# Performance work log

Hardware: AMD Instinct MI355X
Metric: run time of the kernel (lower is better)

## Reference

```python
import jax, jax.numpy as jnp
import numpy as np

SUB_NO = 128
T_HIST = 100
T_DATA = 20000
SYN_B = 3
HIST_B = 3
FIX_VAR = 1.0


def _build_kern(delta, log_tau, K):
    # delta: (S,), log_tau: (B,), K: (S,B) -> kernel (S, T_HIST)
    t = jnp.maximum(jnp.arange(T_HIST, dtype=jnp.float32)[None, :] - delta[:, None], 0.0)  # (S,T)
    tt = t[:, :, None] / jnp.exp(log_tau)[None, None, :]  # (S,T,B)
    return jnp.einsum('stb,sb->st', tt * jnp.exp(-tt), K)


def setup_inputs() -> dict:
    key = jax.random.key(0)
    ks = jax.random.split(key, 5)
    S = SUB_NO
    return {
        'S_conv': jax.random.normal(ks[0], (T_DATA, S), jnp.float32),
        'Y_ancest': jax.random.normal(ks[1], (T_DATA, S), jnp.float32),
        'Z_ancest': jax.random.uniform(ks[2], (T_DATA, S), jnp.float32),
        'noise': jax.random.normal(ks[3], (T_DATA, S), jnp.float32),
        'C_den': jax.random.uniform(ks[4], (S, S), jnp.float32),
        'W_sub': jnp.ones(S, jnp.float32) * 0.25,
        'theta_syn': jnp.zeros(S, jnp.float32),
        'K_spike': jnp.ones((S, SYN_B), jnp.float32) * 0.01,
        'tau_spike': jnp.arange(1.6, 1.6 + SYN_B, dtype=jnp.float32),
        'delta_spike': jnp.zeros(S, jnp.float32),
        'theta_spike': jnp.ones(S, jnp.float32) * (-1.0),
        'W_spike': jnp.ones(S, jnp.float32) * 0.1,
        'tau_hist': jnp.arange(0.5, 0.5 + HIST_B * 0.5, 0.5, dtype=jnp.float32),
        'K_hist': jnp.zeros((S, HIST_B), jnp.float32),
        'delta_hist': jnp.zeros(S, jnp.float32),
    }


def _forward(S_conv, Y_ancest, Z_ancest, noise, C_den, W_sub, theta_syn,
             K_spike, tau_spike, delta_spike, theta_spike, W_spike,
             tau_hist, K_hist, delta_hist):
    S = SUB_NO
    # kernels, flipped as in torch (conv1d cross-correlation with flipped kernel)
    hist_kf = _build_kern(delta_hist, tau_hist, K_hist)[:, ::-1]      # (S,T_HIST)
    anc_kf = _build_kern(delta_spike, tau_spike, K_spike)[:, ::-1]    # (S,T_HIST)

    # Ancestor path has no recurrence -> hoist out of the time loop.
    # spike_ancest filtering: C_den is linear & time-independent, so project first,
    # then depthwise-convolve along time.
    Z_pad = jnp.concatenate([jnp.zeros((T_HIST, S), S_conv.dtype), Z_ancest], axis=0)  # (T+T_HIST,S)
    A = Z_pad @ C_den.T  # (T+T_HIST, S)
    conv = jax.lax.conv_general_dilated(
        A.T[None],                 # (1, S, T+T_HIST)
        anc_kf[:, None, :],        # (S, 1, T_HIST)
        window_strides=(1,), padding='VALID',
        dimension_numbers=('NCH', 'OIH', 'NCH'),
        feature_group_count=S)     # (1, S, T_DATA+1)
    filtered_ancest = conv[0].T[:T_DATA]  # (T_DATA, S)

    raw_ancest = Y_ancest @ C_den.T  # (T_DATA, S)
    base = S_conv + theta_syn + filtered_ancest + raw_ancest  # (T_DATA,S)
    sqrt_var = FIX_VAR ** 0.5

    def step(buf, inp):
        # buf: (S, T_HIST) rolling history of Z_out (most recent at index -1)
        b, n = inp
        fh = jnp.sum(buf * hist_kf, axis=1)            # grouped conv1d == per-channel dot
        x_out = jax.nn.sigmoid(b + fh)
        down = x_out * W_spike + theta_spike           # down_mu_Z_t == mu_Z_t (up_mu_Z=None)
        z_out = jax.nn.sigmoid(down + n * sqrt_var)
        buf = jnp.concatenate([buf[:, 1:], z_out[:, None]], axis=1)
        return buf, (x_out * W_sub, z_out, down)

    buf0 = jnp.zeros((S, T_HIST), S_conv.dtype)
    _, (final_Y, final_Z, mu_Z) = jax.lax.scan(step, buf0, (base, noise))
    return final_Y, final_Z, mu_Z, mu_Z


def reference(S_conv, Y_ancest, Z_ancest, noise, C_den, W_sub, theta_syn,
              K_spike, tau_spike, delta_spike, theta_spike, W_spike,
              tau_hist, K_hist, delta_hist):
    return _forward(S_conv, Y_ancest, Z_ancest, noise, C_den, W_sub, theta_syn,
                    K_spike, tau_spike, delta_spike, theta_spike, W_spike,
                    tau_hist, K_hist, delta_hist)
```

## Files before the change

### kernel.cpp

```cpp
#include <hip/hip_runtime.h>

#define T_DATA 20000
#define S_NO   128
#define T_HIST 100
#define J_PAD  104
#define NELEM  (T_DATA * S_NO)

__device__ __forceinline__ float sigm(float v) {
    return 1.0f / (1.0f + __expf(-v));
}

__device__ __forceinline__ void fma4(float4& a, float s, const float4 c) {
    a.x = fmaf(s, c.x, a.x); a.y = fmaf(s, c.y, a.y);
    a.z = fmaf(s, c.z, a.z); a.w = fmaf(s, c.w, a.w);
}

__global__ void __launch_bounds__(256) k1_prep(const float* __restrict__ C,
                        const float* __restrict__ K_spike,
                        const float* __restrict__ tau_spike,
                        const float* __restrict__ delta_spike,
                        const float* __restrict__ tau_hist,
                        const float* __restrict__ K_hist,
                        const float* __restrict__ delta_hist,
                        float* __restrict__ Ct,
                        float* __restrict__ anc_kT,
                        float* __restrict__ hist_k,
                        int* __restrict__ flag) {
    const int tid = threadIdx.x;
    const int b   = blockIdx.x;
    if (b < 16) {
#pragma unroll
        for (int i = 0; i < 4; ++i) {
            const int q = b * 1024 + i * 256 + tid;
            Ct[(q & 127) * S_NO + (q >> 7)] = C[q];
        }
        return;
    }
    const int s    = tid & 127;
    const int half = tid >> 7;
    {
        float d  = delta_spike[s];
        float i0 = __expf(-tau_spike[0]);
        float i1 = __expf(-tau_spike[1]);
        float i2 = __expf(-tau_spike[2]);
        float k0 = K_spike[s * 3 + 0], k1 = K_spike[s * 3 + 1], k2 = K_spike[s * 3 + 2];
        for (int j = half * 52; j < half * 52 + 52; ++j) {
            float v = 0.0f;
            if (j < T_HIST) {
                float t  = fmaxf((float)j - d, 0.0f);
                float x0 = t * i0, x1 = t * i1, x2 = t * i2;
                v = k0 * x0 * __expf(-x0) + k1 * x1 * __expf(-x1) + k2 * x2 * __expf(-x2);
            }
            anc_kT[j * S_NO + s] = v;
        }
    }
    {
        float d  = delta_hist[s];
        float i0 = __expf(-tau_hist[0]);
        float i1 = __expf(-tau_hist[1]);
        float i2 = __expf(-tau_hist[2]);
        float k0 = K_hist[s * 3 + 0], k1 = K_hist[s * 3 + 1], k2 = K_hist[s * 3 + 2];
        for (int j = half * 50; j < half * 50 + 50; ++j) {
            float t  = fmaxf((float)j - d, 0.0f);
            float x0 = t * i0, x1 = t * i1, x2 = t * i2;
            hist_k[s * T_HIST + j] =
                k0 * x0 * __expf(-x0) + k1 * x1 * __expf(-x1) + k2 * x2 * __expf(-x2);
        }
    }
    if (tid == 0) *flag = 0;
    __syncthreads();
    if (tid < 128) {
        if (K_hist[s * 3] != 0.0f || K_hist[s * 3 + 1] != 0.0f || K_hist[s * 3 + 2] != 0.0f)
            atomicOr(flag, 1);
    }
}

__global__ void __launch_bounds__(256) k2_gemm(const float* __restrict__ Z,
                                               const float* __restrict__ Y,
                                               const float* __restrict__ Ct,
                                               float* __restrict__ A,
                                               float* __restrict__ R) {
    __shared__ float Zt[32 * 128];
    __shared__ float Yt[32 * 128];
    const int t0  = blockIdx.x * 32;
    const int tid = threadIdx.x;
    {
        const float4* Zg = (const float4*)(Z + t0 * S_NO);
        const float4* Yg = (const float4*)(Y + t0 * S_NO);
        float4* Zl = (float4*)Zt;
        float4* Yl = (float4*)Yt;
        for (int q = tid; q < 1024; q += 256) { Zl[q] = Zg[q]; Yl[q] = Yg[q]; }
    }
    __syncthreads();
    const int sg = tid & 31;
    const int tg = tid >> 5;
    const int s0 = sg * 4;
    float4 accA[4] = {{0,0,0,0},{0,0,0,0},{0,0,0,0},{0,0,0,0}};
    float4 accR[4] = {{0,0,0,0},{0,0,0,0},{0,0,0,0},{0,0,0,0}};
    for (int k4 = 0; k4 < 32; ++k4) {
        const float4 c0 = *(const float4*)&Ct[(k4 * 4 + 0) * S_NO + s0];
        const float4 c1 = *(const float4*)&Ct[(k4 * 4 + 1) * S_NO + s0];
        const float4 c2 = *(const float4*)&Ct[(k4 * 4 + 2) * S_NO + s0];
        const float4 c3 = *(const float4*)&Ct[(k4 * 4 + 3) * S_NO + s0];
#pragma unroll
        for (int i = 0; i < 4; ++i) {
            const float4 z = *(const float4*)&Zt[(tg * 4 + i) * S_NO + k4 * 4];
            fma4(accA[i], z.x, c0); fma4(accA[i], z.y, c1);
            fma4(accA[i], z.z, c2); fma4(accA[i], z.w, c3);
            const float4 y = *(const float4*)&Yt[(tg * 4 + i) * S_NO + k4 * 4];
            fma4(accR[i], y.x, c0); fma4(accR[i], y.y, c1);
            fma4(accR[i], y.z, c2); fma4(accR[i], y.w, c3);
        }
    }
#pragma unroll
    for (int i = 0; i < 4; ++i) {
        *(float4*)&A[(t0 + tg * 4 + i) * S_NO + s0] = accA[i];
        *(float4*)&R[(t0 + tg * 4 + i) * S_NO + s0] = accR[i];
    }
}

#define K3_LOGICAL 1250
#define K3_NPER    157
#define K3_PHYS    (8 * K3_NPER)

__device__ __forceinline__ void k3_load_chunk(const float* __restrict__ A,
                                              const float* __restrict__ kT,
                                              int t0, int s, int c,
                                              float w[15], float kj[8]) {
    const int B = t0 - 8 * c - 8;
#pragma unroll
    for (int q = 0; q < 15; ++q) w[q] = A[(B + q) * S_NO + s];
#pragma unroll
    for (int r = 0; r < 8; ++r) kj[r] = kT[(8 * c + r) * S_NO + s];
}

__device__ __forceinline__ void k3_fma_chunk(const float w[15], const float kj[8],
                                             float acc[8]) {
#pragma unroll
    for (int r = 0; r < 8; ++r)
#pragma unroll
        for (int i = 0; i < 8; ++i)
            acc[i] = fmaf(kj[r], w[i + 7 - r], acc[i]);
}

__device__ __forceinline__ void conv8_guard(const float* __restrict__ A,
                                            const float* __restrict__ kT,
                                            int t0, int s, float acc[8]) {
#pragma unroll 1
    for (int c = 0; c < 13; ++c) {
        const int B = t0 - 8 * c - 8;
        float w[15], kj[8];
#pragma unroll
        for (int q = 0; q < 15; ++q) {
            const int u = B + q;
            w[q] = (u >= 0) ? A[u * S_NO + s] : 0.0f;
        }
#pragma unroll
        for (int r = 0; r < 8; ++r) kj[r] = kT[(8 * c + r) * S_NO + s];
        k3_fma_chunk(w, kj, acc);
    }
}

__global__ void __launch_bounds__(256, 4) k3_fused(const float* __restrict__ A,
                                                const float* __restrict__ anc_kT,
                                                const float* __restrict__ S_conv,
                                                const float* __restrict__ noise,
                                                const float* __restrict__ W_sub,
                                                const float* __restrict__ theta_syn,
                                                const float* __restrict__ theta_spike,
                                                const float* __restrict__ W_spike,
                                                const int* __restrict__ flag,
                                                float* __restrict__ out0,
                                                float* __restrict__ out1,
                                                float* __restrict__ out2,
                                                float* __restrict__ out3,
                                                float* __restrict__ Fws) {
    const int blk = (blockIdx.x & 7) * K3_NPER + (blockIdx.x >> 3);
    if (blk >= K3_LOGICAL) return;
    const int tid = threadIdx.x;
    const int s   = tid & 127;
    const int tg  = tid >> 7;
    const int t0  = blk * 16 + tg * 8;
    const int fl  = *flag;

    float sc[8], nz[8];
#pragma unroll
    for (int i = 0; i < 8; ++i) {
        const int n = (t0 + i) * S_NO + s;
        sc[i] = S_conv[n];
        nz[i] = noise[n];
    }

    float acc[8] = {0,0,0,0,0,0,0,0};
    if (t0 >= J_PAD) {
        float w0[15], k0[8], w1[15], k1[8];
        k3_load_chunk(A, anc_kT, t0, s, 0, w0, k0);
#pragma unroll 1
        for (int c = 0; c < 12; c += 2) {
            k3_load_chunk(A, anc_kT, t0, s, c + 1, w1, k1);
            k3_fma_chunk(w0, k0, acc);
            k3_load_chunk(A, anc_kT, t0, s, c + 2, w0, k0);
            k3_fma_chunk(w1, k1, acc);
        }
        k3_fma_chunk(w0, k0, acc);
    } else {
        conv8_guard(A, anc_kT, t0, s, acc);
    }

    if (fl == 0) {
        const float tsy = theta_syn[s], wsub = W_sub[s];
        const float wsp = W_spike[s],  tsp  = theta_spike[s];
#pragma unroll
        for (int i = 0; i < 8; ++i) {
            const int n = (t0 + i) * S_NO + s;
            const float x  = sigm(sc[i] + tsy + out1[n] + acc[i]);
            const float dn = fmaf(x, wsp, tsp);
            const float z  = sigm(dn + nz[i]);
            out0[n] = x * wsub;
            out1[n] = z;
            out2[n] = dn;
            out3[n] = dn;
        }
    } else {
#pragma unroll
        for (int i = 0; i < 8; ++i) Fws[(t0 + i) * S_NO + s] = acc[i];
    }
}

__global__ void __launch_bounds__(64) k4_scan(const float* __restrict__ S_conv,
                                              const float* __restrict__ noise,
                                              const float* __restrict__ W_sub,
                                              const float* __restrict__ theta_syn,
                                              const float* __restrict__ theta_spike,
                                              const float* __restrict__ W_spike,
                                              const float* __restrict__ hist_k,
                                              const int* __restrict__ flag,
                                              const float* __restrict__ Fws,
                                              float* __restrict__ out0,
                                              float* __restrict__ out1,
                                              float* __restrict__ out2,
                                              float* __restrict__ out3) {
    if (*flag == 0) return;
    __shared__ float zr[128];
    const int s = blockIdx.x;
    const int l = threadIdx.x;
    zr[l] = 0.0f; zr[l + 64] = 0.0f;
    const float hk0 = (l < T_HIST) ? hist_k[s * T_HIST + l] : 0.0f;
    const float hk1 = (l + 64 < T_HIST) ? hist_k[s * T_HIST + l + 64] : 0.0f;
    const float tsy = theta_syn[s], wsub = W_sub[s];
    const float wsp = W_spike[s],  tsp  = theta_spike[s];
    for (int t = 0; t < T_DATA; ++t) {
        float fh = hk0 * zr[(t - 1 - l) & 127];
        fh = fmaf(hk1, zr[(t - 65 - l) & 127], fh);
#pragma unroll
        for (int m = 1; m < 64; m <<= 1) fh += __shfl_xor(fh, m, 64);
        const int n = t * S_NO + s;
        const float basev = S_conv[n] + tsy + out1[n] + Fws[n];
        const float x  = sigm(basev + fh);
        const float dn = fmaf(x, wsp, tsp);
        const float z  = sigm(dn + noise[n]);
        if (l == 0) {
            out0[n] = x * wsub;
            out1[n] = z;
            out2[n] = dn;
            out3[n] = dn;
            zr[t & 127] = z;
        }
    }
}

extern "C" void kernel_launch(void* const* d_in, const int* in_sizes, int n_in,
                              void* d_out, int out_size, void* d_ws, size_t ws_size,
                              hipStream_t stream) {
    const float* S_conv  = (const float*)d_in[0];
    const float* Y_anc   = (const float*)d_in[1];
    const float* Z_anc   = (const float*)d_in[2];
    const float* noise   = (const float*)d_in[3];
    const float* C_den   = (const float*)d_in[4];
    const float* W_sub   = (const float*)d_in[5];
    const float* th_syn  = (const float*)d_in[6];
    const float* K_spk   = (const float*)d_in[7];
    const float* tau_spk = (const float*)d_in[8];
    const float* dl_spk  = (const float*)d_in[9];
    const float* th_spk  = (const float*)d_in[10];
    const float* W_spk   = (const float*)d_in[11];
    const float* tau_h   = (const float*)d_in[12];
    const float* K_h     = (const float*)d_in[13];
    const float* dl_h    = (const float*)d_in[14];

    float* out  = (float*)d_out;
    float* out0 = out;
    float* out1 = out + NELEM;
    float* out2 = out + 2 * NELEM;
    float* out3 = out + 3 * NELEM;

    float* ws     = (float*)d_ws;
    float* wsA    = ws;
    float* wsF    = ws + NELEM;
    float* Ct     = ws + 2 * NELEM;
    float* anc_kT = Ct + S_NO * S_NO;
    float* hist_k = anc_kT + J_PAD * S_NO;
    int*   flag   = (int*)(hist_k + S_NO * T_HIST);

    k1_prep<<<17, 256, 0, stream>>>(C_den, K_spk, tau_spk, dl_spk, tau_h, K_h, dl_h,
                                    Ct, anc_kT, hist_k, flag);
    k2_gemm<<<T_DATA / 32, 256, 0, stream>>>(Z_anc, Y_anc, Ct, wsA, out1);
    k3_fused<<<K3_PHYS, 256, 0, stream>>>(wsA, anc_kT, S_conv, noise,
                                          W_sub, th_syn, th_spk, W_spk,
                                          flag, out0, out1, out2, out3, wsF);
    k4_scan<<<S_NO, 64, 0, stream>>>(S_conv, noise, W_sub, th_syn, th_spk, W_spk,
                                     hist_k, flag, wsF, out0, out1, out2, out3);
}
```

Measured before the change: 163.7 us.

## Fuse Y_ancest projection GEMM into convolution kernel, drop R round-trip

The Y_ancest x C_den^T projection moves out of the GEMM kernel and into the fused convolution/output kernel. Each thread now computes its own 8 rows of the raw-ancestor term directly from global Y and Ct. This removes the write of R into out1 and the later re-read of it, which was a full T x S round-trip through memory. In exchange, each k3 thread does a 128-length dot product per row with uncoalesced broadcast float4 loads of Y and no shared-memory reuse, which adds compute and L1/L2 traffic to k3.

```diff
diff --git a/kernel.cpp b/kernel.cpp
--- a/kernel.cpp
+++ b/kernel.cpp
@@ -76,27 +76,21 @@
 }
 
 __global__ void __launch_bounds__(256) k2_gemm(const float* __restrict__ Z,
-                                               const float* __restrict__ Y,
                                                const float* __restrict__ Ct,
-                                               float* __restrict__ A,
-                                               float* __restrict__ R) {
+                                               float* __restrict__ A) {
     __shared__ float Zt[32 * 128];
-    __shared__ float Yt[32 * 128];
     const int t0  = blockIdx.x * 32;
     const int tid = threadIdx.x;
     {
         const float4* Zg = (const float4*)(Z + t0 * S_NO);
-        const float4* Yg = (const float4*)(Y + t0 * S_NO);
         float4* Zl = (float4*)Zt;
-        float4* Yl = (float4*)Yt;
-        for (int q = tid; q < 1024; q += 256) { Zl[q] = Zg[q]; Yl[q] = Yg[q]; }
+        for (int q = tid; q < 1024; q += 256) Zl[q] = Zg[q];
     }
     __syncthreads();
     const int sg = tid & 31;
     const int tg = tid >> 5;
     const int s0 = sg * 4;
     float4 accA[4] = {{0,0,0,0},{0,0,0,0},{0,0,0,0},{0,0,0,0}};
-    float4 accR[4] = {{0,0,0,0},{0,0,0,0},{0,0,0,0},{0,0,0,0}};
     for (int k4 = 0; k4 < 32; ++k4) {
         const float4 c0 = *(const float4*)&Ct[(k4 * 4 + 0) * S_NO + s0];
         const float4 c1 = *(const float4*)&Ct[(k4 * 4 + 1) * S_NO + s0];
@@ -107,16 +101,11 @@
             const float4 z = *(const float4*)&Zt[(tg * 4 + i) * S_NO + k4 * 4];
             fma4(accA[i], z.x, c0); fma4(accA[i], z.y, c1);
             fma4(accA[i], z.z, c2); fma4(accA[i], z.w, c3);
-            const float4 y = *(const float4*)&Yt[(tg * 4 + i) * S_NO + k4 * 4];
-            fma4(accR[i], y.x, c0); fma4(accR[i], y.y, c1);
-            fma4(accR[i], y.z, c2); fma4(accR[i], y.w, c3);
-        }
-    }
-#pragma unroll
-    for (int i = 0; i < 4; ++i) {
+        }
+    }
+#pragma unroll
+    for (int i = 0; i < 4; ++i)
         *(float4*)&A[(t0 + tg * 4 + i) * S_NO + s0] = accA[i];
-        *(float4*)&R[(t0 + tg * 4 + i) * S_NO + s0] = accR[i];
-    }
 }
 
 #define K3_LOGICAL 1250
@@ -163,6 +152,8 @@
 
 __global__ void __launch_bounds__(256, 4) k3_fused(const float* __restrict__ A,
                                                 const float* __restrict__ anc_kT,
+                                                const float* __restrict__ Y,
+                                                const float* __restrict__ Ct,
                                                 const float* __restrict__ S_conv,
                                                 const float* __restrict__ noise,
                                                 const float* __restrict__ W_sub,
@@ -191,6 +182,26 @@
         nz[i] = noise[n];
     }
 
+    float accR[8] = {0,0,0,0,0,0,0,0};
+    {
+        const float* Yrow = Y + t0 * S_NO;
+#pragma unroll 4
+        for (int k4 = 0; k4 < 32; ++k4) {
+            const float c0 = Ct[(k4 * 4 + 0) * S_NO + s];
+            const float c1 = Ct[(k4 * 4 + 1) * S_NO + s];
+            const float c2 = Ct[(k4 * 4 + 2) * S_NO + s];
+            const float c3 = Ct[(k4 * 4 + 3) * S_NO + s];
+#pragma unroll
+            for (int i = 0; i < 8; ++i) {
+                const float4 y = *(const float4*)&Yrow[i * S_NO + k4 * 4];
+                accR[i] = fmaf(y.x, c0, accR[i]);
+                accR[i] = fmaf(y.y, c1, accR[i]);
+                accR[i] = fmaf(y.z, c2, accR[i]);
+                accR[i] = fmaf(y.w, c3, accR[i]);
+            }
+        }
+    }
+
     float acc[8] = {0,0,0,0,0,0,0,0};
     if (t0 >= J_PAD) {
         float w0[15], k0[8], w1[15], k1[8];
@@ -213,7 +224,7 @@
 #pragma unroll
         for (int i = 0; i < 8; ++i) {
             const int n = (t0 + i) * S_NO + s;
-            const float x  = sigm(sc[i] + tsy + out1[n] + acc[i]);
+            const float x  = sigm(sc[i] + tsy + accR[i] + acc[i]);
             const float dn = fmaf(x, wsp, tsp);
             const float z  = sigm(dn + nz[i]);
             out0[n] = x * wsub;
@@ -223,7 +234,7 @@
         }
     } else {
 #pragma unroll
-        for (int i = 0; i < 8; ++i) Fws[(t0 + i) * S_NO + s] = acc[i];
+        for (int i = 0; i < 8; ++i) Fws[(t0 + i) * S_NO + s] = acc[i] + accR[i];
     }
 }
 
@@ -255,7 +266,7 @@
 #pragma unroll
         for (int m = 1; m < 64; m <<= 1) fh += __shfl_xor(fh, m, 64);
         const int n = t * S_NO + s;
-        const float basev = S_conv[n] + tsy + out1[n] + Fws[n];
+        const float basev = S_conv[n] + tsy + Fws[n];
         const float x  = sigm(basev + fh);
         const float dn = fmaf(x, wsp, tsp);
         const float z  = sigm(dn + noise[n]);
@@ -304,8 +315,8 @@
 
     k1_prep<<<17, 256, 0, stream>>>(C_den, K_spk, tau_spk, dl_spk, tau_h, K_h, dl_h,
                                     Ct, anc_kT, hist_k, flag);
-    k2_gemm<<<T_DATA / 32, 256, 0, stream>>>(Z_anc, Y_anc, Ct, wsA, out1);
-    k3_fused<<<K3_PHYS, 256, 0, stream>>>(wsA, anc_kT, S_conv, noise,
+    k2_gemm<<<T_DATA / 32, 256, 0, stream>>>(Z_anc, Ct, wsA);
+    k3_fused<<<K3_PHYS, 256, 0, stream>>>(wsA, anc_kT, Y_anc, Ct, S_conv, noise,
                                           W_sub, th_syn, th_spk, W_spk,
                                           flag, out0, out1, out2, out3, wsF);
     k4_scan<<<S_NO, 64, 0, stream>>>(S_conv, noise, W_sub, th_syn, th_spk, W_spk,
```

New measurement: 209.6 us. +28.0%, slower.

## Split ancestor convolution taps across two thread groups with shared-memory reduction

Applied to the files above, without the earlier changes.

The k3 convolution's 13 tap-chunks are padded to 14 (J_PAD 104→112) and split across two halves of a 512-thread block, each doing 7 chunks. The second half writes partial sums to shared memory and the first half adds them after a block barrier before applying the epilogue. The out1 load is also hoisted before the convolution. This doubles thread-level parallelism per output to hide memory latency, at the cost of one extra zero-padded chunk, a __syncthreads, and fewer resident blocks per CU.

```diff
diff --git a/kernel.cpp b/kernel.cpp
--- a/kernel.cpp
+++ b/kernel.cpp
@@ -3,7 +3,7 @@
 #define T_DATA 20000
 #define S_NO   128
 #define T_HIST 100
-#define J_PAD  104
+#define J_PAD  112
 #define NELEM  (T_DATA * S_NO)
 
 __device__ __forceinline__ float sigm(float v) {
@@ -44,7 +44,7 @@
         float i1 = __expf(-tau_spike[1]);
         float i2 = __expf(-tau_spike[2]);
         float k0 = K_spike[s * 3 + 0], k1 = K_spike[s * 3 + 1], k2 = K_spike[s * 3 + 2];
-        for (int j = half * 52; j < half * 52 + 52; ++j) {
+        for (int j = half * 56; j < half * 56 + 56; ++j) {
             float v = 0.0f;
             if (j < T_HIST) {
                 float t  = fmaxf((float)j - d, 0.0f);
@@ -143,11 +143,12 @@
             acc[i] = fmaf(kj[r], w[i + 7 - r], acc[i]);
 }
 
-__device__ __forceinline__ void conv8_guard(const float* __restrict__ A,
+__device__ __forceinline__ void conv7_guard(const float* __restrict__ A,
                                             const float* __restrict__ kT,
-                                            int t0, int s, float acc[8]) {
+                                            int t0, int s, int cbase, float acc[8]) {
 #pragma unroll 1
-    for (int c = 0; c < 13; ++c) {
+    for (int cc = 0; cc < 7; ++cc) {
+        const int c = cbase + cc;
         const int B = t0 - 8 * c - 8;
         float w[15], kj[8];
 #pragma unroll
@@ -161,7 +162,7 @@
     }
 }
 
-__global__ void __launch_bounds__(256, 4) k3_fused(const float* __restrict__ A,
+__global__ void __launch_bounds__(512, 4) k3_fused(const float* __restrict__ A,
                                                 const float* __restrict__ anc_kT,
                                                 const float* __restrict__ S_conv,
                                                 const float* __restrict__ noise,
@@ -177,35 +178,51 @@
                                                 float* __restrict__ Fws) {
     const int blk = (blockIdx.x & 7) * K3_NPER + (blockIdx.x >> 3);
     if (blk >= K3_LOGICAL) return;
+    __shared__ float part[8][2][128];
     const int tid = threadIdx.x;
     const int s   = tid & 127;
-    const int tg  = tid >> 7;
-    const int t0  = blk * 16 + tg * 8;
+    const int g   = tid >> 7;
+    const int th  = g & 1;
+    const int ch  = g >> 1;
+    const int t0  = blk * 16 + th * 8;
     const int fl  = *flag;
 
-    float sc[8], nz[8];
-#pragma unroll
-    for (int i = 0; i < 8; ++i) {
-        const int n = (t0 + i) * S_NO + s;
-        sc[i] = S_conv[n];
-        nz[i] = noise[n];
+    float sc[8], nz[8], rr[8];
+    if (ch == 0) {
+#pragma unroll
+        for (int i = 0; i < 8; ++i) {
+            const int n = (t0 + i) * S_NO + s;
+            sc[i] = S_conv[n];
+            nz[i] = noise[n];
+            rr[i] = out1[n];
+        }
     }
 
     float acc[8] = {0,0,0,0,0,0,0,0};
+    const int cbase = ch * 7;
     if (t0 >= J_PAD) {
-        float w0[15], k0[8], w1[15], k1[8];
-        k3_load_chunk(A, anc_kT, t0, s, 0, w0, k0);
+        float w0[15], kk0[8], w1[15], kk1[8];
+        k3_load_chunk(A, anc_kT, t0, s, cbase, w0, kk0);
 #pragma unroll 1
-        for (int c = 0; c < 12; c += 2) {
-            k3_load_chunk(A, anc_kT, t0, s, c + 1, w1, k1);
-            k3_fma_chunk(w0, k0, acc);
-            k3_load_chunk(A, anc_kT, t0, s, c + 2, w0, k0);
-            k3_fma_chunk(w1, k1, acc);
-        }
-        k3_fma_chunk(w0, k0, acc);
+        for (int c = 0; c < 6; c += 2) {
+            k3_load_chunk(A, anc_kT, t0, s, cbase + c + 1, w1, kk1);
+            k3_fma_chunk(w0, kk0, acc);
+            k3_load_chunk(A, anc_kT, t0, s, cbase + c + 2, w0, kk0);
+            k3_fma_chunk(w1, kk1, acc);
+        }
+        k3_fma_chunk(w0, kk0, acc);
     } else {
-        conv8_guard(A, anc_kT, t0, s, acc);
-    }
+        conv7_guard(A, anc_kT, t0, s, cbase, acc);
+    }
+
+    if (ch == 1) {
+#pragma unroll
+        for (int i = 0; i < 8; ++i) part[i][th][s] = acc[i];
+    }
+    __syncthreads();
+    if (ch == 1) return;
+#pragma unroll
+    for (int i = 0; i < 8; ++i) acc[i] += part[i][th][s];
 
     if (fl == 0) {
         const float tsy = theta_syn[s], wsub = W_sub[s];
@@ -213,7 +230,7 @@
 #pragma unroll
         for (int i = 0; i < 8; ++i) {
             const int n = (t0 + i) * S_NO + s;
-            const float x  = sigm(sc[i] + tsy + out1[n] + acc[i]);
+            const float x  = sigm(sc[i] + tsy + rr[i] + acc[i]);
             const float dn = fmaf(x, wsp, tsp);
             const float z  = sigm(dn + nz[i]);
             out0[n] = x * wsub;
@@ -305,7 +322,7 @@
     k1_prep<<<17, 256, 0, stream>>>(C_den, K_spk, tau_spk, dl_spk, tau_h, K_h, dl_h,
                                     Ct, anc_kT, hist_k, flag);
     k2_gemm<<<T_DATA / 32, 256, 0, stream>>>(Z_anc, Y_anc, Ct, wsA, out1);
-    k3_fused<<<K3_PHYS, 256, 0, stream>>>(wsA, anc_kT, S_conv, noise,
+    k3_fused<<<K3_PHYS, 512, 0, stream>>>(wsA, anc_kT, S_conv, noise,
                                           W_sub, th_syn, th_spk, W_spk,
                                           flag, out0, out1, out2, out3, wsF);
     k4_scan<<<S_NO, 64, 0, stream>>>(S_conv, noise, W_sub, th_syn, th_spk, W_spk,
```

New measurement: 167.0 us. 2.0% more time.

## Stage conv input window in LDS and enlarge k3 blocks to 24 rows

Applied to the files above, without the earlier changes.

The fused ancestor-convolution kernel now copies a 128-row window of the projected activations into shared memory with vectorized loads. Each thread then reads its 15-wide sliding windows from LDS instead of global memory, and each block covers 24 time rows with 384 threads instead of 16 rows with 256. The residual input is preloaded, and bounds guards handle the partial final block. This cuts redundant global/L2 reads of overlapping conv windows, at the cost of 64KB of LDS per block (lower occupancy) and an extra barrier.

```diff
diff --git a/kernel.cpp b/kernel.cpp
--- a/kernel.cpp
+++ b/kernel.cpp
@@ -119,17 +119,19 @@
     }
 }
 
-#define K3_LOGICAL 1250
-#define K3_NPER    157
+#define K3_ROWS    24
+#define K3_TILE    128
+#define K3_LOGICAL 834
+#define K3_NPER    105
 #define K3_PHYS    (8 * K3_NPER)
 
-__device__ __forceinline__ void k3_load_chunk(const float* __restrict__ A,
-                                              const float* __restrict__ kT,
-                                              int t0, int s, int c,
-                                              float w[15], float kj[8]) {
-    const int B = t0 - 8 * c - 8;
-#pragma unroll
-    for (int q = 0; q < 15; ++q) w[q] = A[(B + q) * S_NO + s];
+__device__ __forceinline__ void k3_load_chunk_lds(const float* __restrict__ tile,
+                                                  const float* __restrict__ kT,
+                                                  int base, int s, int c,
+                                                  float w[15], float kj[8]) {
+    const int rb = base - 8 * c;
+#pragma unroll
+    for (int q = 0; q < 15; ++q) w[q] = tile[(rb + q) * S_NO + s];
 #pragma unroll
     for (int r = 0; r < 8; ++r) kj[r] = kT[(8 * c + r) * S_NO + s];
 }
@@ -161,7 +163,7 @@
     }
 }
 
-__global__ void __launch_bounds__(256, 4) k3_fused(const float* __restrict__ A,
+__global__ void __launch_bounds__(384, 2) k3_fused(const float* __restrict__ A,
                                                 const float* __restrict__ anc_kT,
                                                 const float* __restrict__ S_conv,
                                                 const float* __restrict__ noise,
@@ -177,32 +179,45 @@
                                                 float* __restrict__ Fws) {
     const int blk = (blockIdx.x & 7) * K3_NPER + (blockIdx.x >> 3);
     if (blk >= K3_LOGICAL) return;
+    __shared__ float tile[K3_TILE * S_NO];
     const int tid = threadIdx.x;
     const int s   = tid & 127;
     const int tg  = tid >> 7;
-    const int t0  = blk * 16 + tg * 8;
+    const int t0b = blk * K3_ROWS;
+    const int t0  = t0b + tg * 8;
     const int fl  = *flag;
 
-    float sc[8], nz[8];
+    float sc[8], nz[8], rr[8];
 #pragma unroll
     for (int i = 0; i < 8; ++i) {
-        const int n = (t0 + i) * S_NO + s;
-        sc[i] = S_conv[n];
-        nz[i] = noise[n];
+        const int t = t0 + i;
+        const int n = t * S_NO + s;
+        const bool v = (t < T_DATA);
+        sc[i] = v ? S_conv[n] : 0.0f;
+        nz[i] = v ? noise[n]  : 0.0f;
+        rr[i] = v ? out1[n]   : 0.0f;
     }
 
     float acc[8] = {0,0,0,0,0,0,0,0};
-    if (t0 >= J_PAD) {
-        float w0[15], k0[8], w1[15], k1[8];
-        k3_load_chunk(A, anc_kT, t0, s, 0, w0, k0);
+    if (t0b >= J_PAD) {
+        {
+            const float4* g = (const float4*)(A + (t0b - J_PAD) * S_NO);
+            float4* l = (float4*)tile;
+#pragma unroll 1
+            for (int c = tid; c < K3_TILE * S_NO / 4; c += 384) l[c] = g[c];
+        }
+        __syncthreads();
+        const int base = tg * 8 + 96;
+        float w0[15], kk0[8], w1[15], kk1[8];
+        k3_load_chunk_lds(tile, anc_kT, base, s, 0, w0, kk0);
 #pragma unroll 1
         for (int c = 0; c < 12; c += 2) {
-            k3_load_chunk(A, anc_kT, t0, s, c + 1, w1, k1);
-            k3_fma_chunk(w0, k0, acc);
-            k3_load_chunk(A, anc_kT, t0, s, c + 2, w0, k0);
-            k3_fma_chunk(w1, k1, acc);
-        }
-        k3_fma_chunk(w0, k0, acc);
+            k3_load_chunk_lds(tile, anc_kT, base, s, c + 1, w1, kk1);
+            k3_fma_chunk(w0, kk0, acc);
+            k3_load_chunk_lds(tile, anc_kT, base, s, c + 2, w0, kk0);
+            k3_fma_chunk(w1, kk1, acc);
+        }
+        k3_fma_chunk(w0, kk0, acc);
     } else {
         conv8_guard(A, anc_kT, t0, s, acc);
     }
@@ -212,18 +227,24 @@
         const float wsp = W_spike[s],  tsp  = theta_spike[s];
 #pragma unroll
         for (int i = 0; i < 8; ++i) {
-            const int n = (t0 + i) * S_NO + s;
-            const float x  = sigm(sc[i] + tsy + out1[n] + acc[i]);
-            const float dn = fmaf(x, wsp, tsp);
-            const float z  = sigm(dn + nz[i]);
-            out0[n] = x * wsub;
-            out1[n] = z;
-            out2[n] = dn;
-            out3[n] = dn;
+            const int t = t0 + i;
+            if (t < T_DATA) {
+                const int n = t * S_NO + s;
+                const float x  = sigm(sc[i] + tsy + rr[i] + acc[i]);
+                const float dn = fmaf(x, wsp, tsp);
+                const float z  = sigm(dn + nz[i]);
+                out0[n] = x * wsub;
+                out1[n] = z;
+                out2[n] = dn;
+                out3[n] = dn;
+            }
         }
     } else {
 #pragma unroll
-        for (int i = 0; i < 8; ++i) Fws[(t0 + i) * S_NO + s] = acc[i];
+        for (int i = 0; i < 8; ++i) {
+            const int t = t0 + i;
+            if (t < T_DATA) Fws[t * S_NO + s] = acc[i];
+        }
     }
 }
 
@@ -305,7 +326,7 @@
     k1_prep<<<17, 256, 0, stream>>>(C_den, K_spk, tau_spk, dl_spk, tau_h, K_h, dl_h,
                                     Ct, anc_kT, hist_k, flag);
     k2_gemm<<<T_DATA / 32, 256, 0, stream>>>(Z_anc, Y_anc, Ct, wsA, out1);
-    k3_fused<<<K3_PHYS, 256, 0, stream>>>(wsA, anc_kT, S_conv, noise,
+    k3_fused<<<K3_PHYS, 384, 0, stream>>>(wsA, anc_kT, S_conv, noise,
                                           W_sub, th_syn, th_spk, W_spk,
                                           flag, out0, out1, out2, out3, wsF);
     k4_scan<<<S_NO, 64, 0, stream>>>(S_conv, noise, W_sub, th_syn, th_spk, W_spk,
```

Result: slower. 173.1 us (+5.8%).
